# Performance work log

Hardware: AMD Instinct MI355X
Metric: run time of the kernel (lower is better)

## Reference

```python
import jax, jax.numpy as jnp
import numpy as np

B_, L_ = 1, 1024
D_MODEL, D_INNER, D_XB = 2048, 4096, 1024
D_STATE = 16
DT_RANK = 128
INTER = 8192
EPS = 1e-5
GC = D_INNER // D_STATE   # 256 state groups (each covers D_STATE channels)
REP = D_INNER // D_XB     # 4: repeat_kv expansion factor for x and B


def setup_inputs() -> dict:
    key = jax.random.key(0)
    ks = jax.random.split(key, 8)
    s = 0.02
    return {
        "hidden_states": jax.random.normal(ks[0], (B_, L_, D_MODEL), jnp.float32),
        "rms1_w": jnp.ones((D_MODEL,), jnp.float32),
        "in_proj_w": jax.random.normal(ks[1], (2 * D_INNER + 2 * D_XB + DT_RANK, D_MODEL), jnp.float32) * s,
        "dt_proj_w": jax.random.normal(ks[2], (D_INNER, DT_RANK), jnp.float32) * s,
        "dt_proj_b": jax.random.normal(ks[3], (D_INNER,), jnp.float32) * 0.5 - 4.0,
        "A_log": jnp.tile(jnp.log(jnp.arange(1, D_STATE + 1, dtype=jnp.float32)), (D_INNER, 1)),
        "D_skip": jnp.ones((D_INNER,), jnp.float32),
        "out_proj_w": jax.random.normal(ks[4], (D_MODEL, D_INNER), jnp.float32) * s,
        "rms2_w": jnp.ones((D_MODEL,), jnp.float32),
        "gate_w": jax.random.normal(ks[5], (INTER, D_MODEL), jnp.float32) * s,
        "up_w": jax.random.normal(ks[6], (INTER, D_MODEL), jnp.float32) * s,
        "down_w": jax.random.normal(ks[7], (D_MODEL, INTER), jnp.float32) * s,
    }


def _rmsnorm(x, w):
    return x * jax.lax.rsqrt(jnp.mean(x * x, axis=-1, keepdims=True) + EPS) * w


def _mamba(x, in_proj_w, dt_proj_w, dt_proj_b, A_log, D_skip, out_proj_w):
    b, l, _ = x.shape
    zxbcdt = x @ in_proj_w.T  # (b,l, 2*d_inner + 2*d_xb + dt_rank)
    z = zxbcdt[..., :D_INNER]
    xv = zxbcdt[..., D_INNER:D_INNER + D_XB]
    Bm = zxbcdt[..., D_INNER + D_XB:D_INNER + 2 * D_XB]
    Cm = zxbcdt[..., D_INNER + 2 * D_XB:2 * D_INNER + 2 * D_XB]
    dt_in = zxbcdt[..., 2 * D_INNER + 2 * D_XB:]
    dt = jax.nn.softplus(dt_in @ dt_proj_w.T + dt_proj_b)  # (b,l,d_inner)
    # repeat_kv-style expansion of x and B from d_xb to d_inner (grouped by d_state)
    xg = jnp.repeat(xv.reshape(b, l, D_XB // D_STATE, D_STATE), REP, axis=2)  # (b,l,GC,n)
    Bg = jnp.repeat(Bm.reshape(b, l, D_XB // D_STATE, D_STATE), REP, axis=2)  # (b,l,GC,n)
    Cg = Cm.reshape(b, l, GC, D_STATE)                                        # (b,l,GC,n)
    x_full = xg.reshape(b, l, D_INNER)
    A = -jnp.exp(A_log)                       # (d_inner, n)
    dA = jnp.exp(dt[..., None] * A)           # (b,l,d_inner,n)
    dtx = (dt * x_full).reshape(b, l, GC, D_INNER // GC)  # channels per group == D_STATE here
    dBx = (dtx[..., :, None] * Bg[..., None, :]).reshape(b, l, D_INNER, D_STATE)

    def step(h, inp):
        dA_i, dBx_i, C_i = inp
        h = dA_i * h + dBx_i                  # (b,d_inner,n)
        # channel d in group d // D_STATE shares C of that group
        y = jnp.einsum('bgn,bgcn->bgc', C_i, h.reshape(b, GC, D_INNER // GC, D_STATE))
        return h, y.reshape(b, D_INNER)

    h0 = jnp.zeros((b, D_INNER, D_STATE), x.dtype)
    _, ys = jax.lax.scan(step, h0, (dA.transpose(1, 0, 2, 3), dBx.transpose(1, 0, 2, 3), Cg.transpose(1, 0, 2, 3)))
    y = ys.transpose(1, 0, 2) + D_skip * x_full
    y = y * jax.nn.silu(z)
    return y @ out_proj_w.T


def reference(hidden_states, rms1_w, in_proj_w, dt_proj_w, dt_proj_b, A_log, D_skip, out_proj_w, rms2_w, gate_w, up_w, down_w):
    res = hidden_states
    h = _rmsnorm(hidden_states, rms1_w)
    h = res + _mamba(h, in_proj_w, dt_proj_w, dt_proj_b, A_log, D_skip, out_proj_w)
    res = h
    hn = _rmsnorm(h, rms2_w)
    mlp = (jax.nn.silu(hn @ gate_w.T) * (hn @ up_w.T)) @ down_w.T
    return res + mlp
```

## Files before the change

### kernel.cpp

```cpp
#include <hip/hip_runtime.h>
#include <cstdint>
#include <cstddef>

#define L_SEQ   1024
#define DMODEL  2048
#define DINNER  4096
#define DXB     1024
#define DSTATE  16
#define DTRANK  128
#define INTER   8192
#define ZROW    10368
#define NCHUNK  64
#define CLEN    16

typedef __attribute__((ext_vector_type(8))) short  short8;
typedef __attribute__((ext_vector_type(4))) float  floatx4;
typedef unsigned short ushort_t;

__device__ __forceinline__ unsigned short f2bf(float f) {
  unsigned u = __float_as_uint(f);
  u += 0x7FFFu + ((u >> 16) & 1u);
  return (unsigned short)(u >> 16);
}
__device__ __forceinline__ float bf2f(unsigned short h) {
  return __uint_as_float(((unsigned)h) << 16);
}

__device__ __forceinline__ void gl_lds16(const void* g, void* l) {
  __builtin_amdgcn_global_load_lds(
      (const __attribute__((address_space(1))) unsigned int*)g,
      (__attribute__((address_space(3))) unsigned int*)l,
      16, 0, 0);
}

__global__ void __launch_bounds__(256) cvt_kernel(
    const float* __restrict__ src, ushort_t* __restrict__ dst, int n8)
{
  int idx = blockIdx.x * 256 + threadIdx.x;
  if (idx < n8) {
    const float4* s = (const float4*)src + (size_t)idx * 2;
    float4 v0 = s[0], v1 = s[1];
    union { ushort_t u[8]; uint4 v; } o;
    o.u[0] = f2bf(v0.x); o.u[1] = f2bf(v0.y); o.u[2] = f2bf(v0.z); o.u[3] = f2bf(v0.w);
    o.u[4] = f2bf(v1.x); o.u[5] = f2bf(v1.y); o.u[6] = f2bf(v1.z); o.u[7] = f2bf(v1.w);
    ((uint4*)dst)[idx] = o.v;
  }
}

template <int EPI, bool WF32>
__global__ void __launch_bounds__(256, 2) gemm_ring(
    const ushort_t* __restrict__ A, int lda,
    const ushort_t* __restrict__ W, int ldw,
    float* __restrict__ C, int ldc, int K,
    const float* __restrict__ aux,
    ushort_t* __restrict__ Cb, int col_lo, int ldcb)
{
  constexpr int ASZ = 128 * 32;
  __shared__ alignas(16) ushort_t As[4 * ASZ];
  __shared__ alignas(16) ushort_t Bs[4 * ASZ];

  const int gx = gridDim.x, gy = gridDim.y;
  const int nwg = gx * gy * (int)gridDim.z;
  const int id  = ((int)blockIdx.z * gy + (int)blockIdx.y) * gx + (int)blockIdx.x;
  const int q = nwg >> 3, r = nwg & 7, xc = id & 7, dd = id >> 3;
  const int wg = (xc < r ? xc * (q + 1) : r * (q + 1) + (xc - r) * q) + dd;
  const int bx  = wg % gx;
  const int byz = wg / gx;
  const int by  = byz % gy;
  const int kz  = byz / gy;

  A += (size_t)kz * K;
  W += (size_t)kz * K;
  float* Cz = nullptr;
  if constexpr (WF32) Cz = C + (size_t)kz * gy * 128 * ldc;

  const int m0 = by * 128, n0 = bx * 128;
  const int t = threadIdx.x;
  const int lane = t & 63, wave = t >> 6;
  const int wm = wave & 1, wn = wave >> 1;
  const int lrow = lane & 15, quad = lane >> 4;
  const int chunk = (quad ^ (lrow & 3)) << 3;

  const int srow = wave * 16 + (lane >> 2);
  const int skof = (((lane & 3) ^ ((lane >> 2) & 3)) << 3);

  const ushort_t* gA0 = A + (size_t)(m0 +  0 + srow) * lda + skof;
  const ushort_t* gA1 = A + (size_t)(m0 + 64 + srow) * lda + skof;
  const ushort_t* gW0 = W + (size_t)(n0 +  0 + srow) * ldw + skof;
  const ushort_t* gW1 = W + (size_t)(n0 + 64 + srow) * ldw + skof;
  ushort_t* lA0 = As + wave * 512;
  ushort_t* lA1 = As + 2048 + wave * 512;
  ushort_t* lB0 = Bs + wave * 512;
  ushort_t* lB1 = Bs + 2048 + wave * 512;

  floatx4 zero = {0.f, 0.f, 0.f, 0.f};
  floatx4 acc[4][4];
#pragma unroll
  for (int a = 0; a < 4; ++a)
#pragma unroll
    for (int b = 0; b < 4; ++b) acc[a][b] = zero;

  const int T = K >> 5;

#pragma unroll
  for (int p = 0; p < 3; ++p) {
    const int ko = p * 32, s = p * ASZ;
    gl_lds16(gA0 + ko, lA0 + s);
    gl_lds16(gA1 + ko, lA1 + s);
    gl_lds16(gW0 + ko, lB0 + s);
    gl_lds16(gW1 + ko, lB1 + s);
  }

  for (int tt = 0; tt < T; ++tt) {
    if (tt + 2 < T)      asm volatile("s_waitcnt vmcnt(8)" ::: "memory");
    else if (tt + 1 < T) asm volatile("s_waitcnt vmcnt(4)" ::: "memory");
    else                 asm volatile("s_waitcnt vmcnt(0)" ::: "memory");
    __builtin_amdgcn_s_barrier();
    __builtin_amdgcn_sched_barrier(0);

    if (tt + 3 < T) {
      const int ko = (tt + 3) * 32;
      const int s  = ((tt + 3) & 3) * ASZ;
      gl_lds16(gA0 + ko, lA0 + s);
      gl_lds16(gA1 + ko, lA1 + s);
      gl_lds16(gW0 + ko, lB0 + s);
      gl_lds16(gW1 + ko, lB1 + s);
    }

    const int cs = (tt & 3) * ASZ;
    short8 af[4], bf_[4];
#pragma unroll
    for (int mi = 0; mi < 4; ++mi)
      af[mi] = *(const short8*)&As[cs + (wm * 64 + mi * 16 + lrow) * 32 + chunk];
#pragma unroll
    for (int ni = 0; ni < 4; ++ni)
      bf_[ni] = *(const short8*)&Bs[cs + (wn * 64 + ni * 16 + lrow) * 32 + chunk];
#pragma unroll
    for (int mi = 0; mi < 4; ++mi)
#pragma unroll
      for (int ni = 0; ni < 4; ++ni)
        acc[mi][ni] = __builtin_amdgcn_mfma_f32_16x16x32_bf16(af[mi], bf_[ni], acc[mi][ni], 0, 0, 0);
  }

#pragma unroll
  for (int mi = 0; mi < 4; ++mi)
#pragma unroll
    for (int ni = 0; ni < 4; ++ni)
#pragma unroll
      for (int reg = 0; reg < 4; ++reg) {
        int row = m0 + wm * 64 + mi * 16 + quad * 4 + reg;
        int col = n0 + wn * 64 + ni * 16 + lrow;
        float v = acc[mi][ni][reg];
        if (EPI == 1) {
          v += aux[col];
          v = (v > 20.f) ? v : log1pf(__expf(v));
        }
        if constexpr (WF32)
          Cz[(size_t)row * ldc + col] = v;
        if (Cb != nullptr && col >= col_lo)
          Cb[(size_t)row * ldcb + (col - col_lo)] = f2bf(v);
      }
}

template <int S>
__global__ void __launch_bounds__(256) reduce_add_kernel(
    const float* __restrict__ part, int stride4,
    const float* __restrict__ aux, float* __restrict__ out, int n4)
{
  int idx = blockIdx.x * 256 + threadIdx.x;
  if (idx < n4) {
    float4 v = ((const float4*)aux)[idx];
#pragma unroll
    for (int s = 0; s < S; ++s) {
      float4 p = ((const float4*)part)[(size_t)s * stride4 + idx];
      v.x += p.x; v.y += p.y; v.z += p.z; v.w += p.w;
    }
    ((float4*)out)[idx] = v;
  }
}

__global__ void __launch_bounds__(256) reduce_rms_kernel(
    const float* __restrict__ part, int stride,
    const float* __restrict__ hidden,
    const float* __restrict__ w,
    float* __restrict__ h2, ushort_t* __restrict__ hn)
{
  const int row = blockIdx.x;
  const int c0 = threadIdx.x * 8;
  float4 v0 = *(const float4*)(hidden + (size_t)row * DMODEL + c0);
  float4 v1 = *(const float4*)(hidden + (size_t)row * DMODEL + c0 + 4);
#pragma unroll
  for (int s = 0; s < 4; ++s) {
    const float* p = part + (size_t)s * stride + (size_t)row * DMODEL + c0;
    float4 p0 = *(const float4*)p;
    float4 p1 = *(const float4*)(p + 4);
    v0.x += p0.x; v0.y += p0.y; v0.z += p0.z; v0.w += p0.w;
    v1.x += p1.x; v1.y += p1.y; v1.z += p1.z; v1.w += p1.w;
  }
  *(float4*)(h2 + (size_t)row * DMODEL + c0)     = v0;
  *(float4*)(h2 + (size_t)row * DMODEL + c0 + 4) = v1;
  float ss = v0.x*v0.x + v0.y*v0.y + v0.z*v0.z + v0.w*v0.w
           + v1.x*v1.x + v1.y*v1.y + v1.z*v1.z + v1.w*v1.w;
#pragma unroll
  for (int off = 32; off > 0; off >>= 1) ss += __shfl_down(ss, off);
  __shared__ float red[5];
  const int lane = threadIdx.x & 63, wv = threadIdx.x >> 6;
  if (lane == 0) red[wv] = ss;
  __syncthreads();
  if (threadIdx.x == 0)
    red[4] = rsqrtf((red[0] + red[1] + red[2] + red[3]) / (float)DMODEL + 1e-5f);
  __syncthreads();
  const float scale = red[4];
  float4 w0 = *(const float4*)(w + c0);
  float4 w1 = *(const float4*)(w + c0 + 4);
  union { ushort_t u[8]; uint4 q; } o;
  o.u[0] = f2bf(v0.x * scale * w0.x); o.u[1] = f2bf(v0.y * scale * w0.y);
  o.u[2] = f2bf(v0.z * scale * w0.z); o.u[3] = f2bf(v0.w * scale * w0.w);
  o.u[4] = f2bf(v1.x * scale * w1.x); o.u[5] = f2bf(v1.y * scale * w1.y);
  o.u[6] = f2bf(v1.z * scale * w1.z); o.u[7] = f2bf(v1.w * scale * w1.w);
  *(uint4*)(hn + (size_t)row * DMODEL + c0) = o.q;
}

__global__ void __launch_bounds__(256) rmsnorm_kernel(
    const float* __restrict__ x, const float* __restrict__ w,
    ushort_t* __restrict__ out)
{
  const int row = blockIdx.x;
  const float* xr = x + (size_t)row * DMODEL;
  float ss = 0.f;
#pragma unroll
  for (int c = threadIdx.x * 4; c < DMODEL; c += 256 * 4) {
    float4 v = *(const float4*)(xr + c);
    ss += v.x * v.x + v.y * v.y + v.z * v.z + v.w * v.w;
  }
#pragma unroll
  for (int off = 32; off > 0; off >>= 1) ss += __shfl_down(ss, off);
  __shared__ float red[5];
  const int lane = threadIdx.x & 63, wv = threadIdx.x >> 6;
  if (lane == 0) red[wv] = ss;
  __syncthreads();
  if (threadIdx.x == 0)
    red[4] = rsqrtf((red[0] + red[1] + red[2] + red[3]) / (float)DMODEL + 1e-5f);
  __syncthreads();
  const float scale = red[4];
  ushort_t* orow = out + (size_t)row * DMODEL;
#pragma unroll
  for (int c = threadIdx.x * 4; c < DMODEL; c += 256 * 4) {
    float4 v  = *(const float4*)(xr + c);
    float4 w4 = *(const float4*)(w + c);
    ushort4 o;
    o.x = f2bf(v.x * scale * w4.x); o.y = f2bf(v.y * scale * w4.y);
    o.z = f2bf(v.z * scale * w4.z); o.w = f2bf(v.w * scale * w4.w);
    *(ushort4*)(orow + c) = o;
  }
}

__global__ void __launch_bounds__(256) scan_phase1(
    const float* __restrict__ zx, const float* __restrict__ dt,
    const float* __restrict__ A_log,
    float* __restrict__ hend, float* __restrict__ sdtb)
{
  const int gt = blockIdx.x * 256 + threadIdx.x;
  const int i  = gt & 4095;
  const int c  = gt >> 12;
  const int l0 = c * CLEN;

  float a[16];
  *(float4*)&a[0]  = *(const float4*)(A_log + i * 16 + 0);
  *(float4*)&a[4]  = *(const float4*)(A_log + i * 16 + 4);
  *(float4*)&a[8]  = *(const float4*)(A_log + i * 16 + 8);
  *(float4*)&a[12] = *(const float4*)(A_log + i * 16 + 12);
#pragma unroll
  for (int n = 0; n < 16; ++n) a[n] = -__expf(a[n]);

  float h[16];
#pragma unroll
  for (int n = 0; n < 16; ++n) h[n] = 0.f;
  float sdt = 0.f;

  const int xci = DINNER + ((i >> 6) << 4) + (i & 15);
  const int bci = DINNER + DXB + ((i >> 6) << 4);
  const float* zr = zx + (size_t)l0 * ZROW;
  const float* dr = dt + (size_t)l0 * DINNER + i;

#pragma unroll 4
  for (int l = 0; l < CLEN; ++l) {
    const float* row = zr + l * ZROW;
    const float d = dr[l * DINNER];
    const float x = row[xci];
    float B[16];
    *(float4*)&B[0]  = *(const float4*)(row + bci);
    *(float4*)&B[4]  = *(const float4*)(row + bci + 4);
    *(float4*)&B[8]  = *(const float4*)(row + bci + 8);
    *(float4*)&B[12] = *(const float4*)(row + bci + 12);
    sdt += d;
    const float dtx = d * x;
#pragma unroll
    for (int n = 0; n < 16; ++n)
      h[n] = __expf(d * a[n]) * h[n] + dtx * B[n];
  }

  float* he = hend + ((size_t)c * 65536 + i * 16);
  *(float4*)(he + 0)  = *(float4*)&h[0];
  *(float4*)(he + 4)  = *(float4*)&h[4];
  *(float4*)(he + 8)  = *(float4*)&h[8];
  *(float4*)(he + 12) = *(float4*)&h[12];
  sdtb[c * 4096 + i] = sdt;
}

__global__ void __launch_bounds__(256) scan_phase2(
    const float* __restrict__ hend, const float* __restrict__ sdtb,
    const float* __restrict__ A_log,
    float* __restrict__ hstart)
{
  const int cs = blockIdx.x * 256 + threadIdx.x;
  const float a = -__expf(A_log[cs]);
  const int i  = cs >> 4;
  float H = 0.f;
#pragma unroll 8
  for (int c = 0; c < NCHUNK; ++c) {
    hstart[c * 65536 + cs] = H;
    H = __expf(a * sdtb[c * 4096 + i]) * H + hend[c * 65536 + cs];
  }
}

__global__ void __launch_bounds__(256) scan_phase3(
    const float* __restrict__ zx, const float* __restrict__ dt,
    const float* __restrict__ A_log, const float* __restrict__ D_skip,
    const float* __restrict__ hstart,
    ushort_t* __restrict__ y)
{
  const int gt = blockIdx.x * 256 + threadIdx.x;
  const int i  = gt & 4095;
  const int c  = gt >> 12;
  const int l0 = c * CLEN;

  float a[16];
  *(float4*)&a[0]  = *(const float4*)(A_log + i * 16 + 0);
  *(float4*)&a[4]  = *(const float4*)(A_log + i * 16 + 4);
  *(float4*)&a[8]  = *(const float4*)(A_log + i * 16 + 8);
  *(float4*)&a[12] = *(const float4*)(A_log + i * 16 + 12);
#pragma unroll
  for (int n = 0; n < 16; ++n) a[n] = -__expf(a[n]);
  const float dsk = D_skip[i];

  float h[16];
  const float* hs = hstart + ((size_t)c * 65536 + i * 16);
  *(float4*)&h[0]  = *(const float4*)(hs + 0);
  *(float4*)&h[4]  = *(const float4*)(hs + 4);
  *(float4*)&h[8]  = *(const float4*)(hs + 8);
  *(float4*)&h[12] = *(const float4*)(hs + 12);

  const int xci = DINNER + ((i >> 6) << 4) + (i & 15);
  const int bci = DINNER + DXB + ((i >> 6) << 4);
  const int cci = DINNER + 2 * DXB + (i & ~15);
  const float* zr = zx + (size_t)l0 * ZROW;
  const float* dr = dt + (size_t)l0 * DINNER + i;
  ushort_t*    py = y + (size_t)l0 * DINNER + i;

#pragma unroll 2
  for (int l = 0; l < CLEN; ++l) {
    const float* row = zr + l * ZROW;
    const float d = dr[l * DINNER];
    const float x = row[xci];
    const float z = row[i];
    float B[16], C[16];
    *(float4*)&B[0]  = *(const float4*)(row + bci);
    *(float4*)&B[4]  = *(const float4*)(row + bci + 4);
    *(float4*)&B[8]  = *(const float4*)(row + bci + 8);
    *(float4*)&B[12] = *(const float4*)(row + bci + 12);
    *(float4*)&C[0]  = *(const float4*)(row + cci);
    *(float4*)&C[4]  = *(const float4*)(row + cci + 4);
    *(float4*)&C[8]  = *(const float4*)(row + cci + 8);
    *(float4*)&C[12] = *(const float4*)(row + cci + 12);
    const float dtx = d * x;
    float p0 = 0.f, p1 = 0.f, p2 = 0.f, p3 = 0.f;
#pragma unroll
    for (int n = 0; n < 4; ++n) {
      h[n]      = __expf(d * a[n])      * h[n]      + dtx * B[n];
      h[n + 4]  = __expf(d * a[n + 4])  * h[n + 4]  + dtx * B[n + 4];
      h[n + 8]  = __expf(d * a[n + 8])  * h[n + 8]  + dtx * B[n + 8];
      h[n + 12] = __expf(d * a[n + 12]) * h[n + 12] + dtx * B[n + 12];
      p0 += C[n] * h[n];
      p1 += C[n + 4] * h[n + 4];
      p2 += C[n + 8] * h[n + 8];
      p3 += C[n + 12] * h[n + 12];
    }
    const float p = (p0 + p1) + (p2 + p3);
    const float sz = z / (1.f + __expf(-z));
    py[l * DINNER] = f2bf((p + dsk * x) * sz);
  }
}

__global__ void __launch_bounds__(256) silu_mul2_kernel(
    const ushort_t* __restrict__ gu, ushort_t* __restrict__ out, int n8)
{
  const int idx = blockIdx.x * 256 + threadIdx.x;
  if (idx < n8) {
    const int row = idx >> 10;
    const int j   = (idx & 1023) << 3;
    const ushort_t* gp = gu + (size_t)row * (2 * INTER) + j;
    union { uint4 v; ushort_t u[8]; } gv, uv, ov;
    gv.v = *(const uint4*)gp;
    uv.v = *(const uint4*)(gp + INTER);
#pragma unroll
    for (int jj = 0; jj < 8; ++jj) {
      float gf = bf2f(gv.u[jj]), uf = bf2f(uv.u[jj]);
      ov.u[jj] = f2bf(gf / (1.f + __expf(-gf)) * uf);
    }
    *(uint4*)(out + (size_t)row * INTER + j) = ov.v;
  }
}

extern "C" void kernel_launch(void* const* d_in, const int* in_sizes, int n_in,
                              void* d_out, int out_size, void* d_ws, size_t ws_size,
                              hipStream_t stream)
{
  const float* hidden    = (const float*)d_in[0];
  const float* rms1_w    = (const float*)d_in[1];
  const float* in_proj_w = (const float*)d_in[2];
  const float* dt_proj_w = (const float*)d_in[3];
  const float* dt_proj_b = (const float*)d_in[4];
  const float* A_log     = (const float*)d_in[5];
  const float* D_skip    = (const float*)d_in[6];
  const float* out_proj_w= (const float*)d_in[7];
  const float* rms2_w    = (const float*)d_in[8];
  const float* gate_w    = (const float*)d_in[9];
  const float* up_w      = (const float*)d_in[10];
  const float* down_w    = (const float*)d_in[11];
  float* out = (float*)d_out;

  char* ws = (char*)d_ws;
  ushort_t* h_norm_bf = (ushort_t*)(ws + 0);
  float*    h2        = (float*)   (ws + 4194304);
  ushort_t* hn_bf     = (ushort_t*)(ws + 12582912);
  float*    zxbcdt    = (float*)   (ws + 16777216);
  float*    part1     = (float*)   (ws + 16777216);
  ushort_t* gu_bf     = (ushort_t*)(ws + 16777216);
  ushort_t* hm_bf     = (ushort_t*)(ws + 50331648);
  float*    dtbuf     = (float*)   (ws + 67108864);
  ushort_t* guw_bf    = (ushort_t*)(ws + 67108864);
  float*    part2     = (float*)   (ws + 67108864);
  float*    hend_s    = (float*)   (ws + 83886080);
  float*    hstart_s  = (float*)   (ws + 100663296);
  float*    sdtb_s    = (float*)   (ws + 117440512);
  ushort_t* ybuf_bf   = (ushort_t*)(ws + 118489088);
  ushort_t* dtA_bf    = (ushort_t*)(ws + 126877696);
  ushort_t* wbuf      = (ushort_t*)(ws + 127139840);

  rmsnorm_kernel<<<L_SEQ, 256, 0, stream>>>(hidden, rms1_w, h_norm_bf);
  cvt_kernel<<<(ZROW * DMODEL / 8 + 255) / 256, 256, 0, stream>>>(in_proj_w, wbuf, ZROW * DMODEL / 8);
  gemm_ring<0, true><<<dim3(ZROW / 128, L_SEQ / 128, 1), 256, 0, stream>>>(
      h_norm_bf, DMODEL, wbuf, DMODEL, zxbcdt, ZROW, DMODEL, nullptr,
      dtA_bf, 2 * DINNER + 2 * DXB, DTRANK);
  cvt_kernel<<<(DINNER * DTRANK / 8 + 255) / 256, 256, 0, stream>>>(dt_proj_w, wbuf, DINNER * DTRANK / 8);
  gemm_ring<1, true><<<dim3(DINNER / 128, L_SEQ / 128, 1), 256, 0, stream>>>(
      dtA_bf, DTRANK, wbuf, DTRANK, dtbuf, DINNER, DTRANK, dt_proj_b,
      nullptr, 0, 0);
  scan_phase1<<<1024, 256, 0, stream>>>(zxbcdt, dtbuf, A_log, hend_s, sdtb_s);
  scan_phase2<<<256, 256, 0, stream>>>(hend_s, sdtb_s, A_log, hstart_s);
  scan_phase3<<<1024, 256, 0, stream>>>(zxbcdt, dtbuf, A_log, D_skip, hstart_s, ybuf_bf);
  cvt_kernel<<<(DMODEL * DINNER / 8 + 255) / 256, 256, 0, stream>>>(out_proj_w, wbuf, DMODEL * DINNER / 8);
  gemm_ring<0, true><<<dim3(DMODEL / 128, L_SEQ / 128, 4), 256, 0, stream>>>(
      ybuf_bf, DINNER, wbuf, DINNER, part1, DMODEL, DINNER / 4, nullptr,
      nullptr, 0, 0);
  reduce_rms_kernel<<<L_SEQ, 256, 0, stream>>>(
      part1, L_SEQ * DMODEL, hidden, rms2_w, h2, hn_bf);
  cvt_kernel<<<(INTER * DMODEL / 8 + 255) / 256, 256, 0, stream>>>(gate_w, guw_bf, INTER * DMODEL / 8);
  cvt_kernel<<<(INTER * DMODEL / 8 + 255) / 256, 256, 0, stream>>>(up_w, guw_bf + (size_t)INTER * DMODEL, INTER * DMODEL / 8);
  gemm_ring<0, false><<<dim3(2 * INTER / 128, L_SEQ / 128, 1), 256, 0, stream>>>(
      hn_bf, DMODEL, guw_bf, DMODEL, nullptr, 0, DMODEL, nullptr,
      gu_bf, 0, 2 * INTER);
  silu_mul2_kernel<<<(L_SEQ * INTER / 8) / 256, 256, 0, stream>>>(
      gu_bf, hm_bf, L_SEQ * INTER / 8);
  cvt_kernel<<<(DMODEL * INTER / 8 + 255) / 256, 256, 0, stream>>>(down_w, wbuf, DMODEL * INTER / 8);
  gemm_ring<0, true><<<dim3(DMODEL / 128, L_SEQ / 128, 4), 256, 0, stream>>>(
      hm_bf, INTER, wbuf, INTER, part2, DMODEL, INTER / 4, nullptr,
      nullptr, 0, 0);
  reduce_add_kernel<4><<<(L_SEQ * DMODEL / 4) / 256, 256, 0, stream>>>(
      part2, L_SEQ * DMODEL / 4, h2, out, L_SEQ * DMODEL / 4);
}
```

Measured before the change: 707.8 us.

## Add 256x256-tile MFMA GEMM kernel and use it for the large projections

Adds a new 512-thread GEMM kernel with 256x256 output tiles, 64-wide K steps, double-buffered LDS fed by global_load_lds, an XOR-swizzled LDS layout and s_setprio around the MFMA bursts. It replaces the 128x128 ring GEMM for the in_proj, gate/up, out_proj and down projections. The intent is more data reuse per tile and less global and LDS traffic per MFMA. The out_proj and down GEMMs move to split-K by 8 to keep enough blocks busy, which means larger partial buffers and heavier reductions. The zxbcdt row stride is padded to 10496 so that the column count is a multiple of the tile; the padded tile reads weight rows past the real end of the converted buffer, and the workspace layout is reshuffled to fit the larger buffers.

New measurement: 690.2 us. 1.03x faster.

```diff
diff --git a/kernel.cpp b/kernel.cpp
--- a/kernel.cpp
+++ b/kernel.cpp
@@ -10,6 +10,7 @@
 #define DTRANK  128
 #define INTER   8192
 #define ZROW    10368
+#define ZROWP   10496
 #define NCHUNK  64
 #define CLEN    16
 
@@ -45,6 +46,131 @@
     o.u[4] = f2bf(v1.x); o.u[5] = f2bf(v1.y); o.u[6] = f2bf(v1.z); o.u[7] = f2bf(v1.w);
     ((uint4*)dst)[idx] = o.v;
   }
+}
+
+template <bool WF32>
+__global__ void __launch_bounds__(512, 2) gemm256(
+    const ushort_t* __restrict__ A, int lda,
+    const ushort_t* __restrict__ W, int ldw,
+    float* __restrict__ C, int ldc, int K,
+    ushort_t* __restrict__ Cb, int col_lo, int col_hi, int ldcb)
+{
+  __shared__ alignas(16) ushort_t As[2 * 16384];
+  __shared__ alignas(16) ushort_t Bs[2 * 16384];
+
+  const int gx = gridDim.x, gy = gridDim.y;
+  const int nwg = gx * gy * (int)gridDim.z;
+  const int id  = ((int)blockIdx.z * gy + (int)blockIdx.y) * gx + (int)blockIdx.x;
+  const int q = nwg >> 3, r = nwg & 7, xc = id & 7, dd = id >> 3;
+  const int wg = (xc < r ? xc * (q + 1) : r * (q + 1) + (xc - r) * q) + dd;
+  const int by = wg % gy;
+  const int bx = (wg / gy) % gx;
+  const int kz = wg / (gy * gx);
+
+  const ushort_t* Ap = A + (size_t)kz * K;
+  const ushort_t* Wp = W + (size_t)kz * K;
+  float* Cz = nullptr;
+  if constexpr (WF32) Cz = C + (size_t)kz * gy * 256 * ldc;
+
+  const int m0 = by * 256, n0 = bx * 256;
+  const int tid  = threadIdx.x;
+  const int lane = tid & 63, wave = tid >> 6;
+  const int wm = wave >> 2, wn = wave & 3;
+  const int lrow = lane & 15, quad = lane >> 4;
+  const int l8 = lane >> 3, c8 = lane & 7;
+
+  const ushort_t* gA = Ap + (size_t)(m0 + wave * 32 + l8) * lda + ((c8 ^ l8) << 3);
+  const ushort_t* gW = Wp + (size_t)(n0 + wave * 32 + l8) * ldw + ((c8 ^ l8) << 3);
+  ushort_t* lA = As + wave * 2048;
+  ushort_t* lB = Bs + wave * 2048;
+
+  auto STAGE = [&](int kt, int b) {
+    const ushort_t* ga = gA + kt * 64;
+    const ushort_t* gw = gW + kt * 64;
+    ushort_t* la = lA + b * 16384;
+    ushort_t* lb = lB + b * 16384;
+#pragma unroll
+    for (int j = 0; j < 4; ++j) {
+      gl_lds16(ga + (size_t)j * 8 * lda, la + j * 512);
+      gl_lds16(gw + (size_t)j * 8 * ldw, lb + j * 512);
+    }
+  };
+
+  const int rA0 = (wm * 128 + lrow) * 64;
+  const int rB0 = (wn * 64  + lrow) * 64;
+  const int ck0 = ((quad     ^ (lrow & 7)) << 3);
+  const int ck1 = (((4 | quad) ^ (lrow & 7)) << 3);
+
+  floatx4 acc[8][4];
+#pragma unroll
+  for (int f = 0; f < 8; ++f)
+#pragma unroll
+    for (int n = 0; n < 4; ++n) acc[f][n] = (floatx4){0.f, 0.f, 0.f, 0.f};
+
+  const int T = K >> 6;
+  STAGE(0, 0);
+
+  for (int tt = 0; tt < T; ++tt) {
+    if (tt + 1 < T) {
+      STAGE(tt + 1, (tt + 1) & 1);
+      asm volatile("s_waitcnt vmcnt(8)" ::: "memory");
+    } else {
+      asm volatile("s_waitcnt vmcnt(0)" ::: "memory");
+    }
+    __builtin_amdgcn_s_barrier();
+
+    const int bo = (tt & 1) * 16384;
+    short8 Bfr[4][2], Afr[4][2];
+#pragma unroll
+    for (int n = 0; n < 4; ++n) {
+      Bfr[n][0] = *(const short8*)&Bs[bo + rB0 + n * 1024 + ck0];
+      Bfr[n][1] = *(const short8*)&Bs[bo + rB0 + n * 1024 + ck1];
+    }
+#pragma unroll
+    for (int f = 0; f < 4; ++f) {
+      Afr[f][0] = *(const short8*)&As[bo + rA0 + f * 1024 + ck0];
+      Afr[f][1] = *(const short8*)&As[bo + rA0 + f * 1024 + ck1];
+    }
+    __builtin_amdgcn_s_setprio(1);
+#pragma unroll
+    for (int f = 0; f < 4; ++f)
+#pragma unroll
+      for (int n = 0; n < 4; ++n) {
+        acc[f][n] = __builtin_amdgcn_mfma_f32_16x16x32_bf16(Afr[f][0], Bfr[n][0], acc[f][n], 0, 0, 0);
+        acc[f][n] = __builtin_amdgcn_mfma_f32_16x16x32_bf16(Afr[f][1], Bfr[n][1], acc[f][n], 0, 0, 0);
+      }
+    __builtin_amdgcn_s_setprio(0);
+#pragma unroll
+    for (int f = 0; f < 4; ++f) {
+      Afr[f][0] = *(const short8*)&As[bo + rA0 + (f + 4) * 1024 + ck0];
+      Afr[f][1] = *(const short8*)&As[bo + rA0 + (f + 4) * 1024 + ck1];
+    }
+    __builtin_amdgcn_s_setprio(1);
+#pragma unroll
+    for (int f = 0; f < 4; ++f)
+#pragma unroll
+      for (int n = 0; n < 4; ++n) {
+        acc[f + 4][n] = __builtin_amdgcn_mfma_f32_16x16x32_bf16(Afr[f][0], Bfr[n][0], acc[f + 4][n], 0, 0, 0);
+        acc[f + 4][n] = __builtin_amdgcn_mfma_f32_16x16x32_bf16(Afr[f][1], Bfr[n][1], acc[f + 4][n], 0, 0, 0);
+      }
+    __builtin_amdgcn_s_setprio(0);
+    __builtin_amdgcn_s_barrier();
+  }
+
+#pragma unroll
+  for (int f = 0; f < 8; ++f)
+#pragma unroll
+    for (int n = 0; n < 4; ++n)
+#pragma unroll
+      for (int r = 0; r < 4; ++r) {
+        int row = m0 + wm * 128 + f * 16 + quad * 4 + r;
+        int col = n0 + wn * 64 + n * 16 + lrow;
+        float v = acc[f][n][r];
+        if constexpr (WF32)
+          Cz[(size_t)row * ldc + col] = v;
+        if (Cb != nullptr && col >= col_lo && col < col_hi)
+          Cb[(size_t)row * ldcb + (col - col_lo)] = f2bf(v);
+      }
 }
 
 template <int EPI, bool WF32>
@@ -101,7 +227,6 @@
     for (int b = 0; b < 4; ++b) acc[a][b] = zero;
 
   const int T = K >> 5;
-
 #pragma unroll
   for (int p = 0; p < 3; ++p) {
     const int ko = p * 32, s = p * ASZ;
@@ -179,6 +304,7 @@
   }
 }
 
+template <int S>
 __global__ void __launch_bounds__(256) reduce_rms_kernel(
     const float* __restrict__ part, int stride,
     const float* __restrict__ hidden,
@@ -190,7 +316,7 @@
   float4 v0 = *(const float4*)(hidden + (size_t)row * DMODEL + c0);
   float4 v1 = *(const float4*)(hidden + (size_t)row * DMODEL + c0 + 4);
 #pragma unroll
-  for (int s = 0; s < 4; ++s) {
+  for (int s = 0; s < S; ++s) {
     const float* p = part + (size_t)s * stride + (size_t)row * DMODEL + c0;
     float4 p0 = *(const float4*)p;
     float4 p1 = *(const float4*)(p + 4);
@@ -280,12 +406,12 @@
 
   const int xci = DINNER + ((i >> 6) << 4) + (i & 15);
   const int bci = DINNER + DXB + ((i >> 6) << 4);
-  const float* zr = zx + (size_t)l0 * ZROW;
+  const float* zr = zx + (size_t)l0 * ZROWP;
   const float* dr = dt + (size_t)l0 * DINNER + i;
 
 #pragma unroll 4
   for (int l = 0; l < CLEN; ++l) {
-    const float* row = zr + l * ZROW;
+    const float* row = zr + (size_t)l * ZROWP;
     const float d = dr[l * DINNER];
     const float x = row[xci];
     float B[16];
@@ -354,13 +480,13 @@
   const int xci = DINNER + ((i >> 6) << 4) + (i & 15);
   const int bci = DINNER + DXB + ((i >> 6) << 4);
   const int cci = DINNER + 2 * DXB + (i & ~15);
-  const float* zr = zx + (size_t)l0 * ZROW;
+  const float* zr = zx + (size_t)l0 * ZROWP;
   const float* dr = dt + (size_t)l0 * DINNER + i;
   ushort_t*    py = y + (size_t)l0 * DINNER + i;
 
 #pragma unroll 2
   for (int l = 0; l < CLEN; ++l) {
-    const float* row = zr + l * ZROW;
+    const float* row = zr + (size_t)l * ZROWP;
     const float d = dr[l * DINNER];
     const float x = row[xci];
     const float z = row[i];
@@ -436,23 +562,23 @@
   ushort_t* hn_bf     = (ushort_t*)(ws + 12582912);
   float*    zxbcdt    = (float*)   (ws + 16777216);
   float*    part1     = (float*)   (ws + 16777216);
-  ushort_t* gu_bf     = (ushort_t*)(ws + 16777216);
-  ushort_t* hm_bf     = (ushort_t*)(ws + 50331648);
-  float*    dtbuf     = (float*)   (ws + 67108864);
-  ushort_t* guw_bf    = (ushort_t*)(ws + 67108864);
-  float*    part2     = (float*)   (ws + 67108864);
-  float*    hend_s    = (float*)   (ws + 83886080);
-  float*    hstart_s  = (float*)   (ws + 100663296);
-  float*    sdtb_s    = (float*)   (ws + 117440512);
-  ushort_t* ybuf_bf   = (ushort_t*)(ws + 118489088);
-  ushort_t* dtA_bf    = (ushort_t*)(ws + 126877696);
-  ushort_t* wbuf      = (ushort_t*)(ws + 127139840);
+  ushort_t* guw_bf    = (ushort_t*)(ws + 16777216);
+  float*    part2     = (float*)   (ws + 16777216);
+  ushort_t* gu_bf     = (ushort_t*)(ws + 83886080);
+  ushort_t* hm_bf     = (ushort_t*)(ws + 117440512);
+  float*    dtbuf     = (float*)   (ws + 83886080);
+  float*    hend_s    = (float*)   (ws + 100663296);
+  float*    hstart_s  = (float*)   (ws + 117440512);
+  ushort_t* wbuf      = (ushort_t*)(ws + 134217728);
+  ushort_t* ybuf_bf   = (ushort_t*)(ws + 167772160);
+  float*    sdtb_s    = (float*)   (ws + 176160768);
+  ushort_t* dtA_bf    = (ushort_t*)(ws + 177209344);
 
   rmsnorm_kernel<<<L_SEQ, 256, 0, stream>>>(hidden, rms1_w, h_norm_bf);
   cvt_kernel<<<(ZROW * DMODEL / 8 + 255) / 256, 256, 0, stream>>>(in_proj_w, wbuf, ZROW * DMODEL / 8);
-  gemm_ring<0, true><<<dim3(ZROW / 128, L_SEQ / 128, 1), 256, 0, stream>>>(
-      h_norm_bf, DMODEL, wbuf, DMODEL, zxbcdt, ZROW, DMODEL, nullptr,
-      dtA_bf, 2 * DINNER + 2 * DXB, DTRANK);
+  gemm256<true><<<dim3(ZROWP / 256, L_SEQ / 256, 1), 512, 0, stream>>>(
+      h_norm_bf, DMODEL, wbuf, DMODEL, zxbcdt, ZROWP, DMODEL,
+      dtA_bf, 2 * DINNER + 2 * DXB, ZROW, DTRANK);
   cvt_kernel<<<(DINNER * DTRANK / 8 + 255) / 256, 256, 0, stream>>>(dt_proj_w, wbuf, DINNER * DTRANK / 8);
   gemm_ring<1, true><<<dim3(DINNER / 128, L_SEQ / 128, 1), 256, 0, stream>>>(
       dtA_bf, DTRANK, wbuf, DTRANK, dtbuf, DINNER, DTRANK, dt_proj_b,
@@ -461,22 +587,22 @@
   scan_phase2<<<256, 256, 0, stream>>>(hend_s, sdtb_s, A_log, hstart_s);
   scan_phase3<<<1024, 256, 0, stream>>>(zxbcdt, dtbuf, A_log, D_skip, hstart_s, ybuf_bf);
   cvt_kernel<<<(DMODEL * DINNER / 8 + 255) / 256, 256, 0, stream>>>(out_proj_w, wbuf, DMODEL * DINNER / 8);
-  gemm_ring<0, true><<<dim3(DMODEL / 128, L_SEQ / 128, 4), 256, 0, stream>>>(
-      ybuf_bf, DINNER, wbuf, DINNER, part1, DMODEL, DINNER / 4, nullptr,
-      nullptr, 0, 0);
-  reduce_rms_kernel<<<L_SEQ, 256, 0, stream>>>(
+  gemm256<true><<<dim3(DMODEL / 256, L_SEQ / 256, 8), 512, 0, stream>>>(
+      ybuf_bf, DINNER, wbuf, DINNER, part1, DMODEL, DINNER / 8,
+      nullptr, 0, 0, 0);
+  reduce_rms_kernel<8><<<L_SEQ, 256, 0, stream>>>(
       part1, L_SEQ * DMODEL, hidden, rms2_w, h2, hn_bf);
   cvt_kernel<<<(INTER * DMODEL / 8 + 255) / 256, 256, 0, stream>>>(gate_w, guw_bf, INTER * DMODEL / 8);
   cvt_kernel<<<(INTER * DMODEL / 8 + 255) / 256, 256, 0, stream>>>(up_w, guw_bf + (size_t)INTER * DMODEL, INTER * DMODEL / 8);
-  gemm_ring<0, false><<<dim3(2 * INTER / 128, L_SEQ / 128, 1), 256, 0, stream>>>(
-      hn_bf, DMODEL, guw_bf, DMODEL, nullptr, 0, DMODEL, nullptr,
-      gu_bf, 0, 2 * INTER);
+  gemm256<false><<<dim3(2 * INTER / 256, L_SEQ / 256, 1), 512, 0, stream>>>(
+      hn_bf, DMODEL, guw_bf, DMODEL, nullptr, 0, DMODEL,
+      gu_bf, 0, 2 * INTER, 2 * INTER);
   silu_mul2_kernel<<<(L_SEQ * INTER / 8) / 256, 256, 0, stream>>>(
       gu_bf, hm_bf, L_SEQ * INTER / 8);
   cvt_kernel<<<(DMODEL * INTER / 8 + 255) / 256, 256, 0, stream>>>(down_w, wbuf, DMODEL * INTER / 8);
-  gemm_ring<0, true><<<dim3(DMODEL / 128, L_SEQ / 128, 4), 256, 0, stream>>>(
-      hm_bf, INTER, wbuf, INTER, part2, DMODEL, INTER / 4, nullptr,
-      nullptr, 0, 0);
-  reduce_add_kernel<4><<<(L_SEQ * DMODEL / 4) / 256, 256, 0, stream>>>(
+  gemm256<true><<<dim3(DMODEL / 256, L_SEQ / 256, 8), 512, 0, stream>>>(
+      hm_bf, INTER, wbuf, INTER, part2, DMODEL, INTER / 8,
+      nullptr, 0, 0, 0);
+  reduce_add_kernel<8><<<(L_SEQ * DMODEL / 4) / 256, 256, 0, stream>>>(
       part2, L_SEQ * DMODEL / 4, h2, out, L_SEQ * DMODEL / 4);
 }
```
